# Kernel tuning notes

Measured on AMD Instinct MI355X. Metric: run time of the kernel, lower is better.

## Reference

```python
import jax, jax.numpy as jnp
import numpy as np

# Dimensions
N = 100000      # nodes
E = 500000      # edges
D_IN = 128      # in_channels
H, C = 2, 64    # heads, out_channels per head (out_channels=128)
T = 128         # time_enc.out_channels
MSG = 128       # msg_dim
EDGE_DIM = MSG + T  # 256
SCALE = 1.0 / np.sqrt(C)


def setup_inputs() -> dict:
    key = jax.random.key(0)
    ks = jax.random.split(key, 16)
    s = 0.05
    x = jax.random.normal(ks[0], (N, D_IN), dtype=jnp.float32)
    last_update = jax.random.uniform(ks[1], (N,), dtype=jnp.float32)
    edge_index = jax.random.randint(ks[2], (2, E), 0, N, dtype=jnp.int64)
    t = jax.random.uniform(ks[3], (E,), dtype=jnp.float32) + 1.0  # event times >= last_update typically
    msg = jax.random.normal(ks[4], (E, MSG), dtype=jnp.float32)
    # TimeEncoder: cos(Linear(1, T))
    time_w = jax.random.normal(ks[5], (T, 1), dtype=jnp.float32) * s
    time_b = jax.random.normal(ks[6], (T,), dtype=jnp.float32) * s
    # TransformerConv linear layers (PyG defaults: q/k/v with bias, edge without, skip with bias)
    Wq = jax.random.normal(ks[7], (D_IN, H * C), dtype=jnp.float32) * s
    bq = jnp.zeros((H * C,), dtype=jnp.float32)
    Wk = jax.random.normal(ks[8], (D_IN, H * C), dtype=jnp.float32) * s
    bk = jnp.zeros((H * C,), dtype=jnp.float32)
    Wv = jax.random.normal(ks[9], (D_IN, H * C), dtype=jnp.float32) * s
    bv = jnp.zeros((H * C,), dtype=jnp.float32)
    We = jax.random.normal(ks[10], (EDGE_DIM, H * C), dtype=jnp.float32) * s
    Wskip = jax.random.normal(ks[11], (D_IN, H * C), dtype=jnp.float32) * s
    bskip = jnp.zeros((H * C,), dtype=jnp.float32)
    return dict(x=x, last_update=last_update, edge_index=edge_index, t=t, msg=msg,
                time_w=time_w, time_b=time_b, Wq=Wq, bq=bq, Wk=Wk, bk=bk,
                Wv=Wv, bv=bv, We=We, Wskip=Wskip, bskip=bskip)


def reference(x, last_update, edge_index, t, msg, time_w, time_b,
              Wq, bq, Wk, bk, Wv, bv, We, Wskip, bskip):
    src, dst = edge_index[0], edge_index[1]
    # relative time encoding: cos(Linear(1, T)(rel_t))
    rel_t = t - last_update[src]                                   # [E]
    rel_t_enc = jnp.cos(rel_t[:, None] * time_w[:, 0][None, :] + time_b)  # [E, T]
    edge_attr = jnp.concatenate([rel_t_enc, msg], axis=-1)         # [E, EDGE_DIM]

    # TransformerConv (heads=H, per-head dim C, eval mode so no dropout)
    q = (x @ Wq + bq).reshape(N, H, C)
    k = (x @ Wk + bk).reshape(N, H, C)
    v = (x @ Wv + bv).reshape(N, H, C)
    e = (edge_attr @ We).reshape(E, H, C)

    k_j = k[src] + e                                               # [E, H, C]
    logits = jnp.sum(q[dst] * k_j, axis=-1) * SCALE                # [E, H]

    # segment softmax over destination nodes
    m = jax.ops.segment_max(logits, dst, num_segments=N)           # [N, H]
    p = jnp.exp(logits - m[dst])
    denom = jax.ops.segment_sum(p, dst, num_segments=N)
    alpha = p / (denom[dst] + 1e-16)                               # [E, H]

    msgs = (v[src] + e) * alpha[..., None]                         # [E, H, C]
    out = jax.ops.segment_sum(msgs, dst, num_segments=N).reshape(N, H * C)
    # root/skip connection
    return out + x @ Wskip + bskip
```

## Files before the change

### kernel.cpp

```cpp
#include <hip/hip_runtime.h>
#include <math.h>


#define SCALE_ATTN 0.125f
#define SCAN_CHUNK 512

typedef __attribute__((ext_vector_type(8))) short bf16x8;
typedef __attribute__((ext_vector_type(4))) float f32x4;

union AFrag { bf16x8 v; unsigned short u[8]; };

__device__ __forceinline__ unsigned short f2bf(float f) {
    unsigned int u = __float_as_uint(f);
    u += 0x7fffu + ((u >> 16) & 1u);
    return (unsigned short)(u >> 16);
}
__device__ __forceinline__ float bf2f(unsigned int lo16) {
    return __uint_as_float(lo16 << 16);
}
__device__ __forceinline__ void unpack8(uint4 u, float* f) {
    f[0] = bf2f(u.x & 0xffffu); f[1] = bf2f(u.x >> 16);
    f[2] = bf2f(u.y & 0xffffu); f[3] = bf2f(u.y >> 16);
    f[4] = bf2f(u.z & 0xffffu); f[5] = bf2f(u.z >> 16);
    f[6] = bf2f(u.w & 0xffffu); f[7] = bf2f(u.w >> 16);
}
__device__ __forceinline__ bf16x8 pack2(float4 a, float4 b) {
    AFrag f;
    f.u[0] = f2bf(a.x); f.u[1] = f2bf(a.y); f.u[2] = f2bf(a.z); f.u[3] = f2bf(a.w);
    f.u[4] = f2bf(b.x); f.u[5] = f2bf(b.y); f.u[6] = f2bf(b.z); f.u[7] = f2bf(b.w);
    return f.v;
}

__global__ __launch_bounds__(256) void k_zero(int4* __restrict__ p, int n4)
{
    const int i = blockIdx.x * 256 + threadIdx.x;
    if (i < n4) p[i] = make_int4(0, 0, 0, 0);
}

__global__ __launch_bounds__(512, 4) void k_node_mfma(
    const float4* __restrict__ x4,
    const float* __restrict__ Wq, const float* __restrict__ Wk,
    const float* __restrict__ Wv, const float* __restrict__ Ws,
    const float* __restrict__ bq, const float* __restrict__ bk,
    const float* __restrict__ bv, const float* __restrict__ bs,
    unsigned short* __restrict__ qb, unsigned short* __restrict__ kb,
    unsigned short* __restrict__ vb, unsigned short* __restrict__ skb,
    int N, int numTiles)
{
    __shared__ __align__(16) unsigned short sX[32 * 128];
    const int tid = threadIdx.x;
    const int w = tid >> 6, l = tid & 63;
    const int l15 = l & 15, lg = l >> 4;
    const int mat = w >> 1;
    const int colbase = (w & 1) * 64;

    const float* Wm = (mat == 0) ? Wq : (mat == 1) ? Wk : (mat == 2) ? Wv : Ws;
    const float* bm = (mat == 0) ? bq : (mat == 1) ? bk : (mat == 2) ? bv : bs;
    unsigned short* dst = (mat == 0) ? qb : (mat == 1) ? kb : (mat == 2) ? vb : skb;

    bf16x8 Bf[4][4];
    float bias[4];
    #pragma unroll
    for (int nt = 0; nt < 4; ++nt) {
        const int col = colbase + nt * 16 + l15;
        bias[nt] = bm[col];
        #pragma unroll
        for (int ks = 0; ks < 4; ++ks) {
            AFrag f;
            #pragma unroll
            for (int j = 0; j < 8; ++j)
                f.u[j] = f2bf(Wm[(ks * 32 + lg * 8 + j) * 128 + col]);
            Bf[ks][nt] = f.v;
        }
    }

    for (int tile = blockIdx.x; tile < numTiles; tile += gridDim.x) {
        {
            const int e = tid >> 4, k8 = tid & 15;
            const int row = min(tile * 32 + e, N - 1);
            const float4 a0 = x4[(size_t)row * 32 + k8 * 2];
            const float4 a1 = x4[(size_t)row * 32 + k8 * 2 + 1];
            const int byteoff = (e * 256 + k8 * 16) ^ ((e & 7) << 4);
            *(bf16x8*)((char*)sX + byteoff) = pack2(a0, a1);
        }
        __syncthreads();

        f32x4 acc[2][4];
        #pragma unroll
        for (int m = 0; m < 2; ++m)
            #pragma unroll
            for (int nt = 0; nt < 4; ++nt) acc[m][nt] = (f32x4)(0.f);

        #pragma unroll
        for (int m = 0; m < 2; ++m) {
            const int lrow = m * 16 + l15;
            #pragma unroll
            for (int ks = 0; ks < 4; ++ks) {
                const int byteoff = (lrow * 256 + ks * 64 + lg * 16) ^ ((lrow & 7) << 4);
                const bf16x8 a = *(const bf16x8*)((const char*)sX + byteoff);
                #pragma unroll
                for (int nt = 0; nt < 4; ++nt)
                    acc[m][nt] = __builtin_amdgcn_mfma_f32_16x16x32_bf16(a, Bf[ks][nt], acc[m][nt], 0, 0, 0);
            }
        }

        #pragma unroll
        for (int m = 0; m < 2; ++m) {
            #pragma unroll
            for (int nt = 0; nt < 4; ++nt) {
                const int col = colbase + nt * 16 + l15;
                #pragma unroll
                for (int r = 0; r < 4; ++r) {
                    const int node = tile * 32 + m * 16 + lg * 4 + r;
                    if (node < N)
                        dst[(size_t)node * 128 + col] = f2bf(acc[m][nt][r] + bias[nt]);
                }
            }
        }
        __syncthreads();
    }
}

__global__ __launch_bounds__(512, 4) void k_edge_mfma(
    const float4* __restrict__ msg4,
    const float* __restrict__ relo,
    const float4* __restrict__ tw4, const float4* __restrict__ tb4,
    const float* __restrict__ We,
    unsigned short* __restrict__ ebuf, int E, int numTiles)
{
    __shared__ __align__(16) unsigned short sA[64 * 256];
    const int tid = threadIdx.x;
    const int w = tid >> 6, l = tid & 63;
    const int l15 = l & 15, lg = l >> 4;
    const int cg = w & 3;
    const int mh = w >> 2;

    bf16x8 Bf[8][2];
    #pragma unroll
    for (int ks = 0; ks < 8; ++ks) {
        #pragma unroll
        for (int nt = 0; nt < 2; ++nt) {
            const int col = cg * 32 + nt * 16 + l15;
            AFrag f;
            #pragma unroll
            for (int j = 0; j < 8; ++j)
                f.u[j] = f2bf(We[(ks * 32 + lg * 8 + j) * 128 + col]);
            Bf[ks][nt] = f.v;
        }
    }

    for (int tile = blockIdx.x; tile < numTiles; tile += gridDim.x) {
        const int ebase = tile * 64;

        #pragma unroll
        for (int i = 0; i < 4; ++i) {
            const int U = tid + i * 512;
            const int e = U >> 5, u = U & 31;
            const int er = min(ebase + e, E - 1);
            bf16x8 val;
            if (u < 16) {
                const float rel = relo[er];
                const float4 tww = tw4[u * 2];
                const float4 tw2 = tw4[u * 2 + 1];
                const float4 tbb = tb4[u * 2];
                const float4 tb2 = tb4[u * 2 + 1];
                AFrag c;
                c.u[0] = f2bf(__cosf(fmaf(rel, tww.x, tbb.x)));
                c.u[1] = f2bf(__cosf(fmaf(rel, tww.y, tbb.y)));
                c.u[2] = f2bf(__cosf(fmaf(rel, tww.z, tbb.z)));
                c.u[3] = f2bf(__cosf(fmaf(rel, tww.w, tbb.w)));
                c.u[4] = f2bf(__cosf(fmaf(rel, tw2.x, tb2.x)));
                c.u[5] = f2bf(__cosf(fmaf(rel, tw2.y, tb2.y)));
                c.u[6] = f2bf(__cosf(fmaf(rel, tw2.z, tb2.z)));
                c.u[7] = f2bf(__cosf(fmaf(rel, tw2.w, tb2.w)));
                val = c.v;
            } else {
                const float4 a0 = msg4[(size_t)er * 32 + (u - 16) * 2];
                const float4 a1 = msg4[(size_t)er * 32 + (u - 16) * 2 + 1];
                val = pack2(a0, a1);
            }
            const int byteoff = (e << 9) + ((u ^ (e & 7)) << 4);
            *(bf16x8*)((char*)sA + byteoff) = val;
        }
        __syncthreads();

        f32x4 acc[2][2];
        #pragma unroll
        for (int m = 0; m < 2; ++m)
            #pragma unroll
            for (int nt = 0; nt < 2; ++nt) acc[m][nt] = (f32x4)(0.f);

        #pragma unroll
        for (int ks = 0; ks < 8; ++ks) {
            const int u = ks * 4 + lg;
            #pragma unroll
            for (int m = 0; m < 2; ++m) {
                const int row = mh * 32 + m * 16 + l15;
                const bf16x8 a = *(const bf16x8*)((const char*)sA +
                                   ((row << 9) + ((u ^ (row & 7)) << 4)));
                acc[m][0] = __builtin_amdgcn_mfma_f32_16x16x32_bf16(a, Bf[ks][0], acc[m][0], 0, 0, 0);
                acc[m][1] = __builtin_amdgcn_mfma_f32_16x16x32_bf16(a, Bf[ks][1], acc[m][1], 0, 0, 0);
            }
        }

        #pragma unroll
        for (int m = 0; m < 2; ++m) {
            #pragma unroll
            for (int nt = 0; nt < 2; ++nt) {
                const int col = cg * 32 + nt * 16 + l15;
                #pragma unroll
                for (int r = 0; r < 4; ++r) {
                    const int er = ebase + mh * 32 + m * 16 + (lg << 2) + r;
                    if (er < E) ebuf[(size_t)er * 128 + col] = f2bf(acc[m][nt][r]);
                }
            }
        }
        __syncthreads();
    }
}

__global__ __launch_bounds__(256) void k_hist(
    const int* __restrict__ ei, int* __restrict__ counts, int E)
{
    int i = blockIdx.x * 256 + threadIdx.x;
    if (i < E) atomicAdd(&counts[ei[E + i]], 1);
}

__global__ __launch_bounds__(256) void k_scan_partial(
    const int* __restrict__ counts, int* __restrict__ partial, int N)
{
    const int base = blockIdx.x * SCAN_CHUNK;
    int v = 0;
    for (int i = threadIdx.x; i < SCAN_CHUNK; i += 256) {
        const int idx = base + i;
        if (idx < N) v += counts[idx];
    }
    __shared__ int red[4];
    #pragma unroll
    for (int off = 1; off < 64; off <<= 1) v += __shfl_xor(v, off);
    if ((threadIdx.x & 63) == 0) red[threadIdx.x >> 6] = v;
    __syncthreads();
    if (threadIdx.x == 0) partial[blockIdx.x] = red[0] + red[1] + red[2] + red[3];
}

__global__ __launch_bounds__(256) void k_scan_base(
    const int* __restrict__ partial, int* __restrict__ base, int nb)
{
    __shared__ int tmp[256];
    const int v = (threadIdx.x < nb) ? partial[threadIdx.x] : 0;
    tmp[threadIdx.x] = v;
    __syncthreads();
    for (int off = 1; off < 256; off <<= 1) {
        const int add = (threadIdx.x >= off) ? tmp[threadIdx.x - off] : 0;
        __syncthreads();
        tmp[threadIdx.x] += add;
        __syncthreads();
    }
    if (threadIdx.x < nb) base[threadIdx.x] = tmp[threadIdx.x] - v;
}

__global__ __launch_bounds__(256) void k_scan_final(
    const int* __restrict__ counts, const int* __restrict__ base,
    int* __restrict__ rowptr, int* __restrict__ cursor, int N)
{
    const int i0 = blockIdx.x * SCAN_CHUNK;
    __shared__ int tmp[256];
    const int ia = i0 + threadIdx.x * 2, ib = ia + 1;
    const int v0 = (ia < N) ? counts[ia] : 0;
    const int v1 = (ib < N) ? counts[ib] : 0;
    const int s = v0 + v1;
    tmp[threadIdx.x] = s;
    __syncthreads();
    for (int off = 1; off < 256; off <<= 1) {
        const int add = (threadIdx.x >= off) ? tmp[threadIdx.x - off] : 0;
        __syncthreads();
        tmp[threadIdx.x] += add;
        __syncthreads();
    }
    const int excl = tmp[threadIdx.x] - s + base[blockIdx.x];
    if (ia < N) { rowptr[ia] = excl;      cursor[ia] = excl; }
    if (ib < N) { rowptr[ib] = excl + v0; cursor[ib] = excl + v0; }
}

__global__ __launch_bounds__(256) void k_fill(
    const int* __restrict__ ei, const float* __restrict__ t,
    const float* __restrict__ lu, int* __restrict__ cursor,
    int* __restrict__ perm, int* __restrict__ srcp,
    float* __restrict__ relo, int E)
{
    int i = blockIdx.x * 256 + threadIdx.x;
    if (i < E) {
        const int s = ei[i];
        const int d = ei[E + i];
        const int pos = atomicAdd(&cursor[d], 1);
        perm[pos] = i;
        srcp[pos] = s;
        relo[i] = t[i] - lu[s];
    }
}

__global__ __launch_bounds__(256) void k_agg(
    const int* __restrict__ srcp, const int* __restrict__ perm,
    const int* __restrict__ rowptr, const int* __restrict__ counts,
    const uint4* __restrict__ qb4, const uint4* __restrict__ kb4,
    const uint4* __restrict__ vb4, const uint4* __restrict__ eb4,
    const uint4* __restrict__ skb4, float4* __restrict__ out4, int N)
{
    const int d = blockIdx.x * 4 + (threadIdx.x >> 6);
    if (d >= N) return;
    const int l = threadIdx.x & 63;
    const int s16 = l & 15;
    const int eg = l >> 4;
    const int start = rowptr[d];
    const int deg = counts[d];

    float qf[8];
    unpack8(qb4[(size_t)d * 16 + s16], qf);
    float accf[8] = {0.f, 0.f, 0.f, 0.f, 0.f, 0.f, 0.f, 0.f};
    float denom = 0.f;

    for (int cbase = 0; cbase < deg; cbase += 64) {
        const int clen = min(deg - cbase, 64);
        int mySrc = 0, myEid = 0;
        if (l < clen) {
            mySrc = srcp[start + cbase + l];
            myEid = perm[start + cbase + l];
        }

        #pragma unroll 2
        for (int i = 0; i < clen; i += 4) {
            const int off = i + eg;
            const bool valid = off < clen;
            const int offc = valid ? off : 0;
            const int src = __shfl(mySrc, offc);
            const int eid = __shfl(myEid, offc);
            if (valid) {
                float kf[8], ef[8], vf[8];
                unpack8(kb4[(size_t)src * 16 + s16], kf);
                unpack8(eb4[(size_t)eid * 16 + s16], ef);
                unpack8(vb4[(size_t)src * 16 + s16], vf);
                float s = 0.f;
                #pragma unroll
                for (int j = 0; j < 8; ++j) s = fmaf(qf[j], kf[j] + ef[j], s);
                s += __shfl_xor(s, 1);
                s += __shfl_xor(s, 2);
                s += __shfl_xor(s, 4);
                const float p = __expf(s * SCALE_ATTN);
                denom += p;
                #pragma unroll
                for (int j = 0; j < 8; ++j) accf[j] = fmaf(p, vf[j] + ef[j], accf[j]);
            }
        }
    }
    #pragma unroll
    for (int j = 0; j < 8; ++j) {
        accf[j] += __shfl_xor(accf[j], 16);
        accf[j] += __shfl_xor(accf[j], 32);
    }
    denom += __shfl_xor(denom, 16);
    denom += __shfl_xor(denom, 32);

    if (l < 16) {
        const float inv = 1.f / (denom + 1e-16f);
        float sk[8];
        unpack8(skb4[(size_t)d * 16 + s16], sk);
        float4* o = out4 + (size_t)d * 32 + s16 * 2;
        o[0] = make_float4(fmaf(accf[0], inv, sk[0]), fmaf(accf[1], inv, sk[1]),
                           fmaf(accf[2], inv, sk[2]), fmaf(accf[3], inv, sk[3]));
        o[1] = make_float4(fmaf(accf[4], inv, sk[4]), fmaf(accf[5], inv, sk[5]),
                           fmaf(accf[6], inv, sk[6]), fmaf(accf[7], inv, sk[7]));
    }
}

extern "C" void kernel_launch(void* const* d_in, const int* in_sizes, int n_in,
                              void* d_out, int out_size, void* d_ws, size_t ws_size,
                              hipStream_t stream)
{
    const float* x   = (const float*)d_in[0];
    const float* lu  = (const float*)d_in[1];
    const int*   ei  = (const int*)d_in[2];
    const float* t   = (const float*)d_in[3];
    const float* msg = (const float*)d_in[4];
    const float* tw  = (const float*)d_in[5];
    const float* tb  = (const float*)d_in[6];
    const float* Wq  = (const float*)d_in[7];
    const float* bq  = (const float*)d_in[8];
    const float* Wk  = (const float*)d_in[9];
    const float* bk  = (const float*)d_in[10];
    const float* Wv  = (const float*)d_in[11];
    const float* bv  = (const float*)d_in[12];
    const float* We  = (const float*)d_in[13];
    const float* Wsk = (const float*)d_in[14];
    const float* bsk = (const float*)d_in[15];

    const int N = in_sizes[1];
    const int E = in_sizes[3];
    float* out = (float*)d_out;

    char* ws = (char*)d_ws;
    unsigned short* qb  = (unsigned short*)ws;  ws += (size_t)N * 128 * sizeof(unsigned short);
    unsigned short* kb  = (unsigned short*)ws;  ws += (size_t)N * 128 * sizeof(unsigned short);
    unsigned short* vb  = (unsigned short*)ws;  ws += (size_t)N * 128 * sizeof(unsigned short);
    unsigned short* skb = (unsigned short*)ws;  ws += (size_t)N * 128 * sizeof(unsigned short);
    unsigned short* eb  = (unsigned short*)ws;  ws += (size_t)E * 128 * sizeof(unsigned short);
    int*   counts  = (int*)ws;   ws += (size_t)N * sizeof(int);
    int*   rowptr  = (int*)ws;   ws += (size_t)N * sizeof(int);
    int*   cursor  = (int*)ws;   ws += (size_t)N * sizeof(int);
    int*   perm    = (int*)ws;   ws += (size_t)E * sizeof(int);
    int*   srcp    = (int*)ws;   ws += (size_t)E * sizeof(int);
    float* relo    = (float*)ws; ws += (size_t)E * sizeof(float);
    int*   partial = (int*)ws;   ws += 512 * sizeof(int);
    int*   baseArr = (int*)ws;   ws += 512 * sizeof(int);

    const int nScan = (N + SCAN_CHUNK - 1) / SCAN_CHUNK;

    const int n4 = (N + 3) / 4;
    k_zero<<<(n4 + 255) / 256, 256, 0, stream>>>((int4*)counts, n4);

    k_hist<<<(E + 255) / 256, 256, 0, stream>>>(ei, counts, E);
    k_scan_partial<<<nScan, 256, 0, stream>>>(counts, partial, N);
    k_scan_base<<<1, 256, 0, stream>>>(partial, baseArr, nScan);
    k_scan_final<<<nScan, 256, 0, stream>>>(counts, baseArr, rowptr, cursor, N);
    k_fill<<<(E + 255) / 256, 256, 0, stream>>>(ei, t, lu, cursor, perm, srcp, relo, E);

    const int nTN = (N + 31) / 32;
    k_node_mfma<<<min(nTN, 1024), 512, 0, stream>>>(
        (const float4*)x, Wq, Wk, Wv, Wsk, bq, bk, bv, bsk,
        qb, kb, vb, skb, N, nTN);

    const int nTE = (E + 63) / 64;
    k_edge_mfma<<<min(nTE, 1024), 512, 0, stream>>>(
        (const float4*)msg, relo,
        (const float4*)tw, (const float4*)tb, We, eb, E, nTE);

    k_agg<<<(N + 3) / 4, 256, 0, stream>>>(
        srcp, perm, rowptr, counts,
        (const uint4*)qb, (const uint4*)kb, (const uint4*)vb, (const uint4*)eb,
        (const uint4*)skb, (float4*)out, N);
}
```

Baseline: 355.6 us.

## Double-buffer edge MFMA tiles with register-prefetched msg loads

The edge projection kernel now keeps two LDS tile buffers. It prefetches the next tile's msg rows into registers while MFMAs run on the current tile, then packs them into the alternate buffer, which removes one barrier per iteration. The grid drops from 1024 to 256 persistent blocks and the launch bound allows fewer blocks per CU, since LDS use doubles and register pressure rises. Fewer resident waves may reduce the latency hiding that occupancy used to provide.

```diff
diff --git a/kernel.cpp b/kernel.cpp
--- a/kernel.cpp
+++ b/kernel.cpp
@@ -121,19 +121,22 @@
     }
 }
 
-__global__ __launch_bounds__(512, 4) void k_edge_mfma(
+__global__ __launch_bounds__(512, 2) void k_edge_mfma(
     const float4* __restrict__ msg4,
     const float* __restrict__ relo,
     const float4* __restrict__ tw4, const float4* __restrict__ tb4,
     const float* __restrict__ We,
     unsigned short* __restrict__ ebuf, int E, int numTiles)
 {
-    __shared__ __align__(16) unsigned short sA[64 * 256];
+    __shared__ __align__(16) unsigned short sA[2][64 * 256];
     const int tid = threadIdx.x;
     const int w = tid >> 6, l = tid & 63;
     const int l15 = l & 15, lg = l >> 4;
     const int cg = w & 3;
     const int mh = w >> 2;
+    const int u = tid & 31;
+    const bool isMsg = (u >= 16);
+    const int e0 = tid >> 5;
 
     bf16x8 Bf[8][2];
     #pragma unroll
@@ -149,40 +152,61 @@
         }
     }
 
-    for (int tile = blockIdx.x; tile < numTiles; tile += gridDim.x) {
-        const int ebase = tile * 64;
-
-        #pragma unroll
-        for (int i = 0; i < 4; ++i) {
-            const int U = tid + i * 512;
-            const int e = U >> 5, u = U & 31;
-            const int er = min(ebase + e, E - 1);
-            bf16x8 val;
-            if (u < 16) {
-                const float rel = relo[er];
-                const float4 tww = tw4[u * 2];
-                const float4 tw2 = tw4[u * 2 + 1];
-                const float4 tbb = tb4[u * 2];
-                const float4 tb2 = tb4[u * 2 + 1];
-                AFrag c;
-                c.u[0] = f2bf(__cosf(fmaf(rel, tww.x, tbb.x)));
-                c.u[1] = f2bf(__cosf(fmaf(rel, tww.y, tbb.y)));
-                c.u[2] = f2bf(__cosf(fmaf(rel, tww.z, tbb.z)));
-                c.u[3] = f2bf(__cosf(fmaf(rel, tww.w, tbb.w)));
-                c.u[4] = f2bf(__cosf(fmaf(rel, tw2.x, tb2.x)));
-                c.u[5] = f2bf(__cosf(fmaf(rel, tw2.y, tb2.y)));
-                c.u[6] = f2bf(__cosf(fmaf(rel, tw2.z, tb2.z)));
-                c.u[7] = f2bf(__cosf(fmaf(rel, tw2.w, tb2.w)));
-                val = c.v;
-            } else {
-                const float4 a0 = msg4[(size_t)er * 32 + (u - 16) * 2];
-                const float4 a1 = msg4[(size_t)er * 32 + (u - 16) * 2 + 1];
-                val = pack2(a0, a1);
-            }
-            const int byteoff = (e << 9) + ((u ^ (e & 7)) << 4);
-            *(bf16x8*)((char*)sA + byteoff) = val;
-        }
-        __syncthreads();
+    int tile = blockIdx.x;
+    if (tile >= numTiles) return;
+
+    float4 mr[8];
+
+    #pragma unroll
+    for (int i = 0; i < 4; ++i) {
+        const int er = min(tile * 64 + e0 + i * 16, E - 1);
+        if (isMsg) {
+            mr[i * 2]     = msg4[(size_t)er * 32 + (u - 16) * 2];
+            mr[i * 2 + 1] = msg4[(size_t)er * 32 + (u - 16) * 2 + 1];
+        }
+    }
+    #pragma unroll
+    for (int i = 0; i < 4; ++i) {
+        const int e = e0 + i * 16;
+        const int er = min(tile * 64 + e, E - 1);
+        bf16x8 val;
+        if (isMsg) {
+            val = pack2(mr[i * 2], mr[i * 2 + 1]);
+        } else {
+            const float rel = relo[er];
+            const float4 tww = tw4[u * 2];
+            const float4 tw2 = tw4[u * 2 + 1];
+            const float4 tbb = tb4[u * 2];
+            const float4 tb2 = tb4[u * 2 + 1];
+            AFrag c;
+            c.u[0] = f2bf(__cosf(fmaf(rel, tww.x, tbb.x)));
+            c.u[1] = f2bf(__cosf(fmaf(rel, tww.y, tbb.y)));
+            c.u[2] = f2bf(__cosf(fmaf(rel, tww.z, tbb.z)));
+            c.u[3] = f2bf(__cosf(fmaf(rel, tww.w, tbb.w)));
+            c.u[4] = f2bf(__cosf(fmaf(rel, tw2.x, tb2.x)));
+            c.u[5] = f2bf(__cosf(fmaf(rel, tw2.y, tb2.y)));
+            c.u[6] = f2bf(__cosf(fmaf(rel, tw2.z, tb2.z)));
+            c.u[7] = f2bf(__cosf(fmaf(rel, tw2.w, tb2.w)));
+            val = c.v;
+        }
+        const int byteoff = (e << 9) + ((u ^ (e & 7)) << 4);
+        *(bf16x8*)((char*)&sA[0][0] + byteoff) = val;
+    }
+    __syncthreads();
+
+    int cur = 0;
+    while (tile < numTiles) {
+        const int nxt = tile + (int)gridDim.x;
+        const bool hasNext = nxt < numTiles;
+
+        if (hasNext && isMsg) {
+            #pragma unroll
+            for (int i = 0; i < 4; ++i) {
+                const int er = min(nxt * 64 + e0 + i * 16, E - 1);
+                mr[i * 2]     = msg4[(size_t)er * 32 + (u - 16) * 2];
+                mr[i * 2 + 1] = msg4[(size_t)er * 32 + (u - 16) * 2 + 1];
+            }
+        }
 
         f32x4 acc[2][2];
         #pragma unroll
@@ -192,17 +216,18 @@
 
         #pragma unroll
         for (int ks = 0; ks < 8; ++ks) {
-            const int u = ks * 4 + lg;
+            const int ur = ks * 4 + lg;
             #pragma unroll
             for (int m = 0; m < 2; ++m) {
                 const int row = mh * 32 + m * 16 + l15;
-                const bf16x8 a = *(const bf16x8*)((const char*)sA +
-                                   ((row << 9) + ((u ^ (row & 7)) << 4)));
+                const bf16x8 a = *(const bf16x8*)((const char*)&sA[cur][0] +
+                                   ((row << 9) + ((ur ^ (row & 7)) << 4)));
                 acc[m][0] = __builtin_amdgcn_mfma_f32_16x16x32_bf16(a, Bf[ks][0], acc[m][0], 0, 0, 0);
                 acc[m][1] = __builtin_amdgcn_mfma_f32_16x16x32_bf16(a, Bf[ks][1], acc[m][1], 0, 0, 0);
             }
         }
 
+        const int ebase = tile * 64;
         #pragma unroll
         for (int m = 0; m < 2; ++m) {
             #pragma unroll
@@ -215,7 +240,39 @@
                 }
             }
         }
-        __syncthreads();
+
+        if (hasNext) {
+            #pragma unroll
+            for (int i = 0; i < 4; ++i) {
+                const int e = e0 + i * 16;
+                const int er = min(nxt * 64 + e, E - 1);
+                bf16x8 val;
+                if (isMsg) {
+                    val = pack2(mr[i * 2], mr[i * 2 + 1]);
+                } else {
+                    const float rel = relo[er];
+                    const float4 tww = tw4[u * 2];
+                    const float4 tw2 = tw4[u * 2 + 1];
+                    const float4 tbb = tb4[u * 2];
+                    const float4 tb2 = tb4[u * 2 + 1];
+                    AFrag c;
+                    c.u[0] = f2bf(__cosf(fmaf(rel, tww.x, tbb.x)));
+                    c.u[1] = f2bf(__cosf(fmaf(rel, tww.y, tbb.y)));
+                    c.u[2] = f2bf(__cosf(fmaf(rel, tww.z, tbb.z)));
+                    c.u[3] = f2bf(__cosf(fmaf(rel, tww.w, tbb.w)));
+                    c.u[4] = f2bf(__cosf(fmaf(rel, tw2.x, tb2.x)));
+                    c.u[5] = f2bf(__cosf(fmaf(rel, tw2.y, tb2.y)));
+                    c.u[6] = f2bf(__cosf(fmaf(rel, tw2.z, tb2.z)));
+                    c.u[7] = f2bf(__cosf(fmaf(rel, tw2.w, tb2.w)));
+                    val = c.v;
+                }
+                const int byteoff = (e << 9) + ((u ^ (e & 7)) << 4);
+                *(bf16x8*)((char*)&sA[cur ^ 1][0] + byteoff) = val;
+            }
+        }
+        __syncthreads();
+        cur ^= 1;
+        tile = nxt;
     }
 }
 
@@ -429,7 +486,7 @@
         qb, kb, vb, skb, N, nTN);
 
     const int nTE = (E + 63) / 64;
-    k_edge_mfma<<<min(nTE, 1024), 512, 0, stream>>>(
+    k_edge_mfma<<<min(nTE, 256), 512, 0, stream>>>(
         (const float4*)msg, relo,
         (const float4*)tw, (const float4*)tb, We, eb, E, nTE);
 
```

Result: no change. 354.0 us (-0.4%).
